# Kernel optimization log

Hardware: AMD Instinct MI355X
Metric: run time of the kernel (lower is better)

## Reference

```python
import jax, jax.numpy as jnp
import numpy as np

N = 100000
E = 2000000
LN_EPS = 1e-5


def _ln(x, g, b):
    m = jnp.mean(x, axis=-1, keepdims=True)
    v = jnp.mean((x - m) ** 2, axis=-1, keepdims=True)
    return (x - m) * jax.lax.rsqrt(v + LN_EPS) * g + b


def _gcn_conv(x, W, b, row, col, n_nodes):
    xw = x @ W  # [N, out_dim]
    deg = jax.ops.segment_sum(jnp.ones((row.shape[0],), xw.dtype), row, num_segments=n_nodes) + 1.0
    dinv = jax.lax.rsqrt(deg)
    norm = dinv[row] * dinv[col]  # [E]
    msg = xw[col] * norm[:, None]  # gather + scale, [E, out_dim]
    agg = jax.ops.segment_sum(msg, row, num_segments=n_nodes)
    self_loop = xw * (dinv * dinv)[:, None]
    return agg + self_loop + b


def setup_inputs() -> dict:
    key = jax.random.key(0)
    ks = jax.random.split(key, 32)
    s = 0.05
    d = dict(
        coords=jax.random.normal(ks[0], (N, 2), jnp.float32),
        features=jax.random.normal(ks[1], (N, 3), jnp.float32),
        edge_index=jax.random.randint(ks[2], (2, E), 0, N, jnp.int32),
        # spatial encoder FFN: 2->128, two hidden 128->128 (relu+LN), last 128->128 (relu)
        fw0=jax.random.normal(ks[3], (2, 128), jnp.float32) * s,
        fb0=jnp.zeros((128,), jnp.float32),
        fg0=jnp.ones((128,), jnp.float32),
        fe0=jnp.zeros((128,), jnp.float32),
        fw1=jax.random.normal(ks[4], (128, 128), jnp.float32) * s,
        fb1=jnp.zeros((128,), jnp.float32),
        fg1=jnp.ones((128,), jnp.float32),
        fe1=jnp.zeros((128,), jnp.float32),
        fw2=jax.random.normal(ks[5], (128, 128), jnp.float32) * s,
        fb2=jnp.zeros((128,), jnp.float32),
        fg2=jnp.ones((128,), jnp.float32),
        fe2=jnp.zeros((128,), jnp.float32),
        fw3=jax.random.normal(ks[6], (128, 128), jnp.float32) * s,
        fb3=jnp.zeros((128,), jnp.float32),
        # dec: 128->64->32->16 with tanh between
        dw0=jax.random.normal(ks[7], (128, 64), jnp.float32) * s,
        db0=jnp.zeros((64,), jnp.float32),
        dw1=jax.random.normal(ks[8], (64, 32), jnp.float32) * s,
        db1=jnp.zeros((32,), jnp.float32),
        dw2=jax.random.normal(ks[9], (32, 16), jnp.float32) * s,
        db2=jnp.zeros((16,), jnp.float32),
        # GCN convs: (3+16)->64, 64->64; fc 64->1
        cw1=jax.random.normal(ks[10], (19, 64), jnp.float32) * s,
        cb1=jnp.zeros((64,), jnp.float32),
        cw2=jax.random.normal(ks[11], (64, 64), jnp.float32) * s,
        cb2=jnp.zeros((64,), jnp.float32),
        ow=jax.random.normal(ks[12], (64, 1), jnp.float32) * s,
        ob=jnp.zeros((1,), jnp.float32),
    )
    return d


def reference(coords, features, edge_index,
              fw0, fb0, fg0, fe0, fw1, fb1, fg1, fe1, fw2, fb2, fg2, fe2, fw3, fb3,
              dw0, db0, dw1, db1, dw2, db2,
              cw1, cb1, cw2, cb2, ow, ob):
    # positional encoder FFN (dropout disabled / eval mode)
    h = _ln(jax.nn.relu(coords @ fw0 + fb0), fg0, fe0)
    h = _ln(jax.nn.relu(h @ fw1 + fb1), fg1, fe1)
    h = _ln(jax.nn.relu(h @ fw2 + fb2), fg2, fe2)
    h = jax.nn.relu(h @ fw3 + fb3)
    # decoder to emb_dim
    emb = jnp.tanh(h @ dw0 + db0)
    emb = jnp.tanh(emb @ dw1 + db1)
    emb = emb @ dw2 + db2  # [N, 16]
    x = jnp.concatenate([features, emb], axis=-1)  # [N, 19]
    row, col = edge_index[0], edge_index[1]
    h1 = jax.nn.relu(_gcn_conv(x, cw1, cb1, row, col, x.shape[0]))
    h2 = _gcn_conv(h1, cw2, cb2, row, col, x.shape[0])
    out = h2 @ ow + ob  # [N, 1]
    return out
```

## Files before the change

### kernel.cpp

```cpp
#include <hip/hip_runtime.h>
#include <hip/hip_bf16.h>
#include <math.h>

#define TM 64
#define XROW 64
#define NSEG 8

typedef float v2f __attribute__((ext_vector_type(2)));
typedef float f32x4 __attribute__((ext_vector_type(4)));
typedef __bf16 bf16x8 __attribute__((ext_vector_type(8)));
typedef unsigned short u16x8 __attribute__((ext_vector_type(8)));
typedef unsigned int uint_t;
typedef unsigned short ushort_t;

__device__ __forceinline__ v2f fma2(v2f a, v2f b, v2f c) {
    return __builtin_elementwise_fma(a, b, c);
}
__device__ __forceinline__ v2f splat2(float s) { return (v2f){s, s}; }
__device__ __forceinline__ v2f max02(v2f a) {
    return (v2f){fmaxf(a.x, 0.0f), fmaxf(a.y, 0.0f)};
}
__device__ __forceinline__ uint_t pack_bf16(float lo, float hi) {
    uint_t r;
    asm volatile("v_cvt_pk_bf16_f32 %0, %1, %2" : "=v"(r) : "v"(lo), "v"(hi));
    return r;
}
__device__ __forceinline__ float bf16_f(ushort_t u) {
    union { uint_t i; float f; } c; c.i = ((uint_t)u) << 16; return c.f;
}
__device__ __forceinline__ float blo(uint_t u) {
    union { uint_t i; float f; } c; c.i = u << 16; return c.f;
}
__device__ __forceinline__ float bhi(uint_t u) {
    union { uint_t i; float f; } c; c.i = u & 0xffff0000u; return c.f;
}

__device__ __forceinline__ int aaddr(int node, int feat) {
    return (node * 256 + feat * 2) ^ ((node & 15) << 4);
}

__global__ void prepw3_kernel(const float* __restrict__ W1, const float* __restrict__ W2,
                              const float* __restrict__ W3, ushort_t* __restrict__ out,
                              const float* __restrict__ cw2, const float* __restrict__ cb2,
                              const float* __restrict__ ow, const float* __restrict__ ob,
                              float* __restrict__ wb) {
    if (blockIdx.x == 384) {
        int i = threadIdx.x;
        if (i < 64) {
            float a = 0.f;
            for (int j = 0; j < 64; j++) a += cw2[i * 64 + j] * ow[j];
            wb[i] = a;
        }
        if (i == 0) {
            float bb = 0.f;
            for (int j = 0; j < 64; j++) bb += cb2[j] * ow[j];
            wb[64] = bb + ob[0];
        }
        return;
    }
    int gid = blockIdx.x * 256 + threadIdx.x;
    int layer = gid >> 15;
    int idx   = gid & 32767;
    const float* W = (layer == 0) ? W1 : (layer == 1) ? W2 : W3;
    int j    = idx & 7;
    int lane = (idx >> 3) & 63;
    int rest = idx >> 9;
    int cb   = rest & 7;
    int r2   = rest >> 3;
    int kk   = r2 & 3;
    int h    = r2 >> 2;
    int k = kk * 32 + (lane >> 4) * 8 + j;
    int n = cb * 16 + (lane & 15);
    float wv = W[k * 128 + n];
    ushort_t hi = (ushort_t)pack_bf16(wv, wv);
    ushort_t v;
    if (h == 0) v = hi;
    else {
        float res = wv - bf16_f(hi);
        v = (ushort_t)pack_bf16(res, res);
    }
    out[(size_t)layer * 32768 + idx] = v;
}

__global__ __launch_bounds__(256, 5) void ffn_kernel(
    const float* __restrict__ coords, const float* __restrict__ features,
    const float* __restrict__ dinv,
    const float* __restrict__ fw0, const float* __restrict__ fb0,
    const float* __restrict__ fg0, const float* __restrict__ fe0,
    const ushort_t* __restrict__ wswz,
    const float* __restrict__ fb1, const float* __restrict__ fg1, const float* __restrict__ fe1,
    const float* __restrict__ fb2, const float* __restrict__ fg2, const float* __restrict__ fe2,
    const float* __restrict__ fb3,
    const float* __restrict__ dw0, const float* __restrict__ db0,
    const float* __restrict__ dw1, const float* __restrict__ db1,
    const float* __restrict__ dw2, const float* __restrict__ db2,
    char* __restrict__ xsb, int n_nodes)
{
    __shared__ __align__(16) char abuf[16384];
    __shared__ __align__(16) ushort_t tbuf[128][64];

    const int t    = threadIdx.x;
    const int lane = t & 63;
    const int w    = __builtin_amdgcn_readfirstlane(t >> 6);
    const int jw   = w * 32;
    const int n0   = blockIdx.x * TM;

    int g = n0 + lane;
    if (g >= n_nodes) g = n_nodes - 1;

    {
        float* ps1 = (float*)tbuf;
        float* ps2 = ((float*)tbuf) + 256;
        v2f acc[16];
        float2 c = *(const float2*)&coords[(size_t)g * 2];
        v2f cx = splat2(c.x), cy = splat2(c.y);
        #pragma unroll
        for (int q = 0; q < 16; q++) {
            int j = jw + 2 * q;
            v2f w0 = *(const v2f*)&fw0[j];
            v2f w1 = *(const v2f*)&fw0[128 + j];
            v2f bb = *(const v2f*)&fb0[j];
            acc[q] = max02(fma2(cx, w0, fma2(cy, w1, bb)));
        }
        float s1 = 0.f, s2 = 0.f;
        #pragma unroll
        for (int q = 0; q < 16; q++) {
            s1 += acc[q].x + acc[q].y;
            s2 += acc[q].x * acc[q].x + acc[q].y * acc[q].y;
        }
        ps1[w * 64 + lane] = s1; ps2[w * 64 + lane] = s2;
        __syncthreads();
        float t1 = ps1[lane] + ps1[64 + lane] + ps1[128 + lane] + ps1[192 + lane];
        float t2 = ps2[lane] + ps2[64 + lane] + ps2[128 + lane] + ps2[192 + lane];
        float mean = t1 * (1.0f / 128.0f);
        float var  = t2 * (1.0f / 128.0f) - mean * mean;
        float inv  = rsqrtf(var + 1e-5f);
        v2f mean2 = splat2(mean), inv2 = splat2(inv);
        #pragma unroll
        for (int q = 0; q < 16; q++) {
            int j = jw + 2 * q;
            v2f gm = *(const v2f*)&fg0[j];
            v2f bt = *(const v2f*)&fe0[j];
            v2f o = fma2((acc[q] - mean2) * inv2, gm, bt);
            *(uint_t*)(abuf + aaddr(lane, j)) = pack_bf16(o.x, o.y);
        }
        __syncthreads();
    }

    auto mfma_layer = [&](const ushort_t* Wb, const float* __restrict__ bias) {
        f32x4 acc[2][4] = {};
        #pragma unroll
        for (int kk = 0; kk < 4; kk++) {
            bf16x8 B[2][2];
            #pragma unroll
            for (int cb2 = 0; cb2 < 2; cb2++) {
                int cb = 2 * w + cb2;
                #pragma unroll
                for (int h = 0; h < 2; h++) {
                    const ushort_t* p = Wb + (size_t)(((h * 4 + kk) * 8 + cb) * 64 + lane) * 8;
                    B[cb2][h] = *(const bf16x8*)p;
                }
            }
            #pragma unroll
            for (int rb = 0; rb < 4; rb++) {
                int node = rb * 16 + (lane & 15);
                bf16x8 A = *(const bf16x8*)(abuf + aaddr(node, kk * 32 + (lane >> 4) * 8));
                #pragma unroll
                for (int cb2 = 0; cb2 < 2; cb2++) {
                    acc[cb2][rb] = __builtin_amdgcn_mfma_f32_16x16x32_bf16(A, B[cb2][0], acc[cb2][rb], 0, 0, 0);
                    acc[cb2][rb] = __builtin_amdgcn_mfma_f32_16x16x32_bf16(A, B[cb2][1], acc[cb2][rb], 0, 0, 0);
                }
            }
        }
        __syncthreads();
        float bv0 = bias[jw + (lane & 15)];
        float bv1 = bias[jw + 16 + (lane & 15)];
        #pragma unroll
        for (int cb2 = 0; cb2 < 2; cb2++) {
            int col = jw + cb2 * 16 + (lane & 15);
            float bv = cb2 ? bv1 : bv0;
            #pragma unroll
            for (int rb = 0; rb < 4; rb++) {
                #pragma unroll
                for (int r = 0; r < 4; r++) {
                    float v = fmaxf(acc[cb2][rb][r] + bv, 0.0f);
                    int node = rb * 16 + (lane >> 4) * 4 + r;
                    *(ushort_t*)(abuf + aaddr(node, col)) = (ushort_t)pack_bf16(v, v);
                }
            }
        }
        __syncthreads();
    };

    auto ln_pass = [&](const float* __restrict__ gam, const float* __restrict__ bet) {
        int node = t >> 2;
        int part = t & 3;
        float vals[32];
        float s1 = 0.f, s2 = 0.f;
        #pragma unroll
        for (int q = 0; q < 4; q++) {
            int f0 = part * 32 + q * 8;
            u16x8 u = *(const u16x8*)(abuf + aaddr(node, f0));
            #pragma unroll
            for (int i = 0; i < 8; i++) {
                float v = bf16_f(u[i]);
                vals[q * 8 + i] = v;
                s1 += v; s2 += v * v;
            }
        }
        s1 += __shfl_xor(s1, 1); s1 += __shfl_xor(s1, 2);
        s2 += __shfl_xor(s2, 1); s2 += __shfl_xor(s2, 2);
        float mean = s1 * (1.0f / 128.0f);
        float var  = s2 * (1.0f / 128.0f) - mean * mean;
        float inv  = rsqrtf(var + 1e-5f);
        #pragma unroll
        for (int q = 0; q < 4; q++) {
            int f0 = part * 32 + q * 8;
            uint_t ov[4];
            #pragma unroll
            for (int p = 0; p < 4; p++) {
                v2f gm = *(const v2f*)&gam[f0 + 2 * p];
                v2f bt = *(const v2f*)&bet[f0 + 2 * p];
                float a = (vals[q * 8 + 2 * p]     - mean) * inv * gm.x + bt.x;
                float b = (vals[q * 8 + 2 * p + 1] - mean) * inv * gm.y + bt.y;
                ov[p] = pack_bf16(a, b);
            }
            uint4 uv = make_uint4(ov[0], ov[1], ov[2], ov[3]);
            *(uint4*)(abuf + aaddr(node, f0)) = uv;
        }
        __syncthreads();
    };

    mfma_layer(wswz,         fb1); ln_pass(fg1, fe1);
    mfma_layer(wswz + 32768, fb2); ln_pass(fg2, fe2);
    mfma_layer(wswz + 65536, fb3);

    {
        #pragma unroll
        for (int q = 0; q < 4; q++) {
            int f0 = jw + q * 8;
            u16x8 u = *(const u16x8*)(abuf + aaddr(lane, f0));
            #pragma unroll
            for (int i = 0; i < 8; i++) tbuf[f0 + i][lane] = u[i];
        }
        __syncthreads();
    }

    {
        const float2* src = (const float2*)dw0;
        uint_t* dst = (uint_t*)abuf;
        #pragma unroll
        for (int q = 0; q < 16; q++) {
            int i = q * 256 + t;
            float2 v = src[i];
            dst[i] = pack_bf16(v.x, v.y);
        }
        __syncthreads();
    }

    {
        const int j16 = w * 16;
        v2f d0[8];
        #pragma unroll
        for (int q = 0; q < 8; q++) d0[q] = *(const v2f*)&db0[j16 + 2 * q];
        const uint4* wd = (const uint4*)abuf;
        #pragma unroll 4
        for (int k = 0; k < 128; k++) {
            v2f av = splat2(bf16_f(tbuf[k][lane]));
            uint4 u0 = wd[k * 8 + w * 2];
            uint4 u1 = wd[k * 8 + w * 2 + 1];
            d0[0] = fma2(av, (v2f){blo(u0.x), bhi(u0.x)}, d0[0]);
            d0[1] = fma2(av, (v2f){blo(u0.y), bhi(u0.y)}, d0[1]);
            d0[2] = fma2(av, (v2f){blo(u0.z), bhi(u0.z)}, d0[2]);
            d0[3] = fma2(av, (v2f){blo(u0.w), bhi(u0.w)}, d0[3]);
            d0[4] = fma2(av, (v2f){blo(u1.x), bhi(u1.x)}, d0[4]);
            d0[5] = fma2(av, (v2f){blo(u1.y), bhi(u1.y)}, d0[5]);
            d0[6] = fma2(av, (v2f){blo(u1.z), bhi(u1.z)}, d0[6]);
            d0[7] = fma2(av, (v2f){blo(u1.w), bhi(u1.w)}, d0[7]);
        }
        #pragma unroll
        for (int q = 0; q < 8; q++) d0[q] = (v2f){tanhf(d0[q].x), tanhf(d0[q].y)};
        __syncthreads();
        #pragma unroll
        for (int q = 0; q < 8; q++) {
            uint_t r = pack_bf16(d0[q].x, d0[q].y);
            tbuf[j16 + 2 * q][lane]     = (ushort_t)r;
            tbuf[j16 + 2 * q + 1][lane] = (ushort_t)(r >> 16);
        }
        __syncthreads();
    }

    {
        const int j8 = w * 8;
        v2f d1[4];
        #pragma unroll
        for (int q = 0; q < 4; q++) d1[q] = *(const v2f*)&db1[j8 + 2 * q];
        #pragma unroll 4
        for (int k = 0; k < 64; k++) {
            v2f av = splat2(bf16_f(tbuf[k][lane]));
            const v2f* W2 = (const v2f*)(dw1 + k * 32 + j8);
            #pragma unroll
            for (int q = 0; q < 4; q++) d1[q] = fma2(av, W2[q], d1[q]);
        }
        #pragma unroll
        for (int q = 0; q < 4; q++) d1[q] = (v2f){tanhf(d1[q].x), tanhf(d1[q].y)};
        __syncthreads();
        #pragma unroll
        for (int q = 0; q < 4; q++) {
            uint_t r = pack_bf16(d1[q].x, d1[q].y);
            tbuf[j8 + 2 * q][lane]     = (ushort_t)r;
            tbuf[j8 + 2 * q + 1][lane] = (ushort_t)(r >> 16);
        }
        __syncthreads();
    }

    {
        const int j4 = w * 4;
        v2f d2[2];
        #pragma unroll
        for (int q = 0; q < 2; q++) d2[q] = *(const v2f*)&db2[j4 + 2 * q];
        #pragma unroll 4
        for (int k = 0; k < 32; k++) {
            v2f av = splat2(bf16_f(tbuf[k][lane]));
            const v2f* W2 = (const v2f*)(dw2 + k * 16 + j4);
            d2[0] = fma2(av, W2[0], d2[0]);
            d2[1] = fma2(av, W2[1], d2[1]);
        }
        __syncthreads();
        #pragma unroll
        for (int q = 0; q < 2; q++) {
            uint_t r = pack_bf16(d2[q].x, d2[q].y);
            tbuf[j4 + 2 * q][lane]     = (ushort_t)r;
            tbuf[j4 + 2 * q + 1][lane] = (ushort_t)(r >> 16);
        }
        __syncthreads();
    }

    {
        const int nn = t & 63;
        const int jg = t >> 6;
        int gg = n0 + nn;
        if (gg < n_nodes && jg < 3) {
            float dgg = dinv[gg];
            char* rp = xsb + (size_t)gg * XROW;
            if (jg == 0) {
                float4 f;
                f.x = features[(size_t)gg * 3 + 0] * dgg;
                f.y = features[(size_t)gg * 3 + 1] * dgg;
                f.z = features[(size_t)gg * 3 + 2] * dgg;
                f.w = 0.0f;
                *(float4*)rp = f;
            } else {
                int e0 = (jg - 1) * 8;
                uint_t u[4];
                #pragma unroll
                for (int p = 0; p < 4; p++) {
                    float lo = bf16_f(tbuf[e0 + 2 * p][nn]) * dgg;
                    float hi = bf16_f(tbuf[e0 + 2 * p + 1][nn]) * dgg;
                    u[p] = pack_bf16(lo, hi);
                }
                uint4 uv = make_uint4(u[0], u[1], u[2], u[3]);
                *(uint4*)(rp + 16 + (jg - 1) * 16) = uv;
            }
        }
    }
}

__global__ void deg8_kernel(const int* __restrict__ row, int* __restrict__ cnt8,
                            int E_, int Nn) {
    int s = blockIdx.x & (NSEG - 1);
    int* cs = cnt8 + (size_t)s * Nn;
    int e4 = (blockIdx.x * blockDim.x + threadIdx.x) * 4;
    if (e4 + 3 < E_) {
        int4 r = *(const int4*)&row[e4];
        atomicAdd(&cs[r.x], 1); atomicAdd(&cs[r.y], 1);
        atomicAdd(&cs[r.z], 1); atomicAdd(&cs[r.w], 1);
    } else {
        for (int e = e4; e < E_; e++) atomicAdd(&cs[row[e]], 1);
    }
}

__global__ void scan1_kernel(const int* __restrict__ in, int* __restrict__ out,
                             int* __restrict__ bsum, int n) {
    __shared__ int tmp[256];
    int t = threadIdx.x, b = blockIdx.x;
    int base = b * 2048 + t * 8;
    int v[8]; int s = 0;
    #pragma unroll
    for (int q = 0; q < 8; q++) {
        int idx = base + q;
        v[q] = (idx < n) ? in[idx] : 0;
        s += v[q];
    }
    tmp[t] = s; __syncthreads();
    #pragma unroll
    for (int d = 1; d < 256; d <<= 1) {
        int add = (t >= d) ? tmp[t - d] : 0;
        __syncthreads();
        tmp[t] += add;
        __syncthreads();
    }
    int run = tmp[t] - s;
    #pragma unroll
    for (int q = 0; q < 8; q++) {
        int idx = base + q;
        if (idx < n) out[idx] = run;
        run += v[q];
    }
    if (t == 255) bsum[b] = tmp[t];
}

__global__ void scan2_kernel(int* __restrict__ bsum, int B) {
    __shared__ int tmp[512];
    int t = threadIdx.x;
    tmp[t] = (t < B) ? bsum[t] : 0; __syncthreads();
    #pragma unroll
    for (int d = 1; d < 512; d <<= 1) {
        int add = (t >= d) ? tmp[t - d] : 0;
        __syncthreads();
        tmp[t] += add;
        __syncthreads();
    }
    if (t < B) bsum[t] = tmp[t];
}

__global__ void scanfix_dinv_kernel(int* __restrict__ data, const int* __restrict__ bsum,
                                    const int* __restrict__ cnt8, float* __restrict__ dinv,
                                    int n, int Nn) {
    int i = blockIdx.x * 256 + threadIdx.x;
    if (i < n) {
        int b = i >> 11;
        if (b > 0) data[i] += bsum[b - 1];
    }
    if (i < Nn) {
        int s = 0;
        #pragma unroll
        for (int q = 0; q < NSEG; q++) s += cnt8[(size_t)q * Nn + i];
        dinv[i] = rsqrtf((float)s + 1.0f);
    }
}

__global__ void scatter_kernel(const int* __restrict__ row, const int* __restrict__ col,
                               int* __restrict__ fill8, int* __restrict__ es,
                               int E_, int Nn) {
    int s = blockIdx.x & (NSEG - 1);
    int* fs = fill8 + (size_t)s * Nn;
    int e4 = (blockIdx.x * blockDim.x + threadIdx.x) * 4;
    if (e4 + 3 < E_) {
        int4 r = *(const int4*)&row[e4];
        int4 c = *(const int4*)&col[e4];
        es[atomicAdd(&fs[r.x], 1)] = c.x;
        es[atomicAdd(&fs[r.y], 1)] = c.y;
        es[atomicAdd(&fs[r.z], 1)] = c.z;
        es[atomicAdd(&fs[r.w], 1)] = c.w;
    } else {
        for (int e = e4; e < E_; e++) {
            int p = atomicAdd(&fs[row[e]], 1);
            es[p] = col[e];
        }
    }
}

__global__ __launch_bounds__(256) void node1g_kernel(
    const int* __restrict__ fill8, const int* __restrict__ cnt8, const int* __restrict__ es,
    const float* __restrict__ dinv, const char* __restrict__ xsb,
    const float* __restrict__ cw1, const float* __restrict__ cb1,
    const float* __restrict__ wb, float* __restrict__ ss, int n)
{
    __shared__ float w[19 * 64];
    __shared__ float bbs[64];
    __shared__ float wes[64];
    for (int i = threadIdx.x; i < 19 * 64; i += 256) w[i] = cw1[i];
    for (int i = threadIdx.x; i < 64; i += 256) { bbs[i] = cb1[i]; wes[i] = wb[i]; }
    __syncthreads();
    const int t  = threadIdx.x;
    const int oc = t & 7;
    const int i  = blockIdx.x * 32 + (t >> 3);
    if (i >= n) return;
    const float di = dinv[i];

    float af[19];
    #pragma unroll
    for (int q = 0; q < 19; q++) af[q] = 0.f;

    auto addrow = [&](const char* rp) {
        float4 F = *(const float4*)rp;
        uint4 U0 = *(const uint4*)(rp + 16);
        uint4 U1 = *(const uint4*)(rp + 32);
        af[0] += F.x; af[1] += F.y; af[2] += F.z;
        af[3]  += blo(U0.x); af[4]  += bhi(U0.x);
        af[5]  += blo(U0.y); af[6]  += bhi(U0.y);
        af[7]  += blo(U0.z); af[8]  += bhi(U0.z);
        af[9]  += blo(U0.w); af[10] += bhi(U0.w);
        af[11] += blo(U1.x); af[12] += bhi(U1.x);
        af[13] += blo(U1.y); af[14] += bhi(U1.y);
        af[15] += blo(U1.z); af[16] += bhi(U1.z);
        af[17] += blo(U1.w); af[18] += bhi(U1.w);
    };

    if (oc == 0) addrow(xsb + (size_t)i * XROW);
    const int end = fill8[(size_t)oc * n + i];
    const int dgs = cnt8[(size_t)oc * n + i];
    for (int e = end - dgs; e < end; e++) {
        int c = es[e];
        addrow(xsb + (size_t)c * XROW);
    }

    float a19[19];
    #pragma unroll
    for (int q = 0; q < 19; q++) {
        float v = af[q];
        v += __shfl_xor(v, 1);
        v += __shfl_xor(v, 2);
        v += __shfl_xor(v, 4);
        a19[q] = v * di;
    }

    const int j0 = oc * 8;
    v2f am[4];
    const v2f* w2  = (const v2f*)w;
    const v2f* bb2 = (const v2f*)bbs;
    #pragma unroll
    for (int q = 0; q < 4; q++) am[q] = bb2[j0 / 2 + q];
    #pragma unroll
    for (int k = 0; k < 19; k++) {
        v2f v = splat2(a19[k]);
        #pragma unroll
        for (int q = 0; q < 4; q++) am[q] = fma2(v, w2[k * 32 + j0 / 2 + q], am[q]);
    }
    const v2f* we2 = (const v2f*)wes;
    v2f sv2 = {0.f, 0.f};
    #pragma unroll
    for (int q = 0; q < 4; q++) sv2 = fma2(max02(am[q]), we2[j0 / 2 + q], sv2);
    float sv = sv2.x + sv2.y;
    sv += __shfl_xor(sv, 1);
    sv += __shfl_xor(sv, 2);
    sv += __shfl_xor(sv, 4);
    if (oc == 0) ss[i] = di * sv;
}

__global__ __launch_bounds__(256) void outg_kernel(
    const int* __restrict__ fill8, const int* __restrict__ cnt8, const int* __restrict__ es,
    const float* __restrict__ dinv, const float* __restrict__ ss,
    const float* __restrict__ wb, float* __restrict__ out, int n)
{
    const int t  = threadIdx.x;
    const int oc = t & 7;
    const int i  = blockIdx.x * 32 + (t >> 3);
    if (i >= n) return;
    const int end = fill8[(size_t)oc * n + i];
    const int dgs = cnt8[(size_t)oc * n + i];
    float sum = (oc == 0) ? ss[i] : 0.f;
    for (int e = end - dgs; e < end; e++) {
        int c = es[e];
        sum += ss[c];
    }
    sum += __shfl_xor(sum, 1);
    sum += __shfl_xor(sum, 2);
    sum += __shfl_xor(sum, 4);
    if (oc == 0) out[i] = wb[64] + dinv[i] * sum;
}

extern "C" void kernel_launch(void* const* d_in, const int* in_sizes, int n_in,
                              void* d_out, int out_size, void* d_ws, size_t ws_size,
                              hipStream_t stream) {
    const float* coords   = (const float*)d_in[0];
    const float* features = (const float*)d_in[1];
    const int*   eidx     = (const int*)d_in[2];
    const float* fw0 = (const float*)d_in[3];
    const float* fb0 = (const float*)d_in[4];
    const float* fg0 = (const float*)d_in[5];
    const float* fe0 = (const float*)d_in[6];
    const float* fw1 = (const float*)d_in[7];
    const float* fb1 = (const float*)d_in[8];
    const float* fg1 = (const float*)d_in[9];
    const float* fe1 = (const float*)d_in[10];
    const float* fw2 = (const float*)d_in[11];
    const float* fb2 = (const float*)d_in[12];
    const float* fg2 = (const float*)d_in[13];
    const float* fe2 = (const float*)d_in[14];
    const float* fw3 = (const float*)d_in[15];
    const float* fb3 = (const float*)d_in[16];
    const float* dw0 = (const float*)d_in[17];
    const float* db0 = (const float*)d_in[18];
    const float* dw1 = (const float*)d_in[19];
    const float* db1 = (const float*)d_in[20];
    const float* dw2 = (const float*)d_in[21];
    const float* db2 = (const float*)d_in[22];
    const float* cw1 = (const float*)d_in[23];
    const float* cb1 = (const float*)d_in[24];
    const float* cw2 = (const float*)d_in[25];
    const float* cb2 = (const float*)d_in[26];
    const float* ow  = (const float*)d_in[27];
    const float* ob  = (const float*)d_in[28];
    float* out = (float*)d_out;

    const int Nn = in_sizes[0] / 2;
    const int E_ = in_sizes[2] / 2;
    const int n8 = NSEG * Nn;
    const int NBS = (n8 + 2047) / 2048;
    const int NO = (Nn * 8 + 255) / 256;
    const int NT = (Nn + TM - 1) / TM;
    const int NE = (E_ / 4 + 255) / 256;

    char* ws = (char*)d_ws;
    size_t o = 0;
    char*  xsb   = (char*) (ws + o); o += (size_t)Nn * XROW;
    int*   cnt8  = (int*)  (ws + o); o += (size_t)n8 * sizeof(int);
    int*   fill8 = (int*)  (ws + o); o += (size_t)n8 * sizeof(int);
    int*   bsum  = (int*)  (ws + o); o += 512 * sizeof(int);
    float* dinv  = (float*)(ws + o); o += (size_t)Nn * sizeof(float);
    float* ssb   = (float*)(ws + o); o += (size_t)Nn * sizeof(float);
    int*   es    = (int*)  (ws + o); o += (size_t)E_ * sizeof(int);
    float* wb    = (float*)(ws + o); o += 80 * sizeof(float);
    o = (o + 15) & ~(size_t)15;
    ushort_t* wswz = (ushort_t*)(ws + o); o += 3 * 32768 * sizeof(ushort_t);

    hipMemsetAsync(cnt8, 0, (size_t)n8 * sizeof(int), stream);

    prepw3_kernel<<<385, 256, 0, stream>>>(fw1, fw2, fw3, wswz, cw2, cb2, ow, ob, wb);

    deg8_kernel<<<NE, 256, 0, stream>>>(eidx, cnt8, E_, Nn);
    scan1_kernel<<<NBS, 256, 0, stream>>>(cnt8, fill8, bsum, n8);
    scan2_kernel<<<1, 512, 0, stream>>>(bsum, NBS);
    scanfix_dinv_kernel<<<(n8 + 255) / 256, 256, 0, stream>>>(fill8, bsum, cnt8, dinv, n8, Nn);
    scatter_kernel<<<NE, 256, 0, stream>>>(eidx, eidx + E_, fill8, es, E_, Nn);

    ffn_kernel<<<NT, 256, 0, stream>>>(
        coords, features, dinv,
        fw0, fb0, fg0, fe0,
        wswz,
        fb1, fg1, fe1, fb2, fg2, fe2, fb3,
        dw0, db0,
        dw1, db1, dw2, db2, xsb, Nn);

    node1g_kernel<<<NO, 256, 0, stream>>>(fill8, cnt8, es, dinv, xsb, cw1, cb1, wb, ssb, Nn);
    outg_kernel<<<NO, 256, 0, stream>>>(fill8, cnt8, es, dinv, ssb, wb, out, Nn);
}
```

Before: 409.0 us.

## Merge independent kernels so degree/scatter blocks overlap weight prep and FFN

The degree-count kernel is folded into the weight-swizzle prep kernel, and the CSR scatter kernel is folded into the FFN kernel, with a block-index split choosing which role each block plays. This removes two launches and lets the atomic-bound edge work run alongside the MFMA-bound FFN tiles instead of serialising on the stream. The fused FFN kernel's launch bound drops from 5 to 4 blocks per CU, which may change register allocation and occupancy for the FFN path.

Result: faster. 375.0 us (median of 2 runs) (-8.3%).

```diff
diff --git a/kernel.cpp b/kernel.cpp
--- a/kernel.cpp
+++ b/kernel.cpp
@@ -39,12 +39,29 @@
     return (node * 256 + feat * 2) ^ ((node & 15) << 4);
 }
 
-__global__ void prepw3_kernel(const float* __restrict__ W1, const float* __restrict__ W2,
-                              const float* __restrict__ W3, ushort_t* __restrict__ out,
-                              const float* __restrict__ cw2, const float* __restrict__ cb2,
-                              const float* __restrict__ ow, const float* __restrict__ ob,
-                              float* __restrict__ wb) {
-    if (blockIdx.x == 384) {
+__global__ void deg8_prep_kernel(const int* __restrict__ row, int* __restrict__ cnt8,
+                                 int E_, int Nn, int NE,
+                                 const float* __restrict__ W1, const float* __restrict__ W2,
+                                 const float* __restrict__ W3, ushort_t* __restrict__ outw,
+                                 const float* __restrict__ cw2, const float* __restrict__ cb2,
+                                 const float* __restrict__ ow, const float* __restrict__ ob,
+                                 float* __restrict__ wb) {
+    int bid = blockIdx.x;
+    if (bid < NE) {
+        int s = bid & (NSEG - 1);
+        int* cs = cnt8 + (size_t)s * Nn;
+        int e4 = (bid * 256 + threadIdx.x) * 4;
+        if (e4 + 3 < E_) {
+            int4 r = *(const int4*)&row[e4];
+            atomicAdd(&cs[r.x], 1); atomicAdd(&cs[r.y], 1);
+            atomicAdd(&cs[r.z], 1); atomicAdd(&cs[r.w], 1);
+        } else {
+            for (int e = e4; e < E_; e++) atomicAdd(&cs[row[e]], 1);
+        }
+        return;
+    }
+    int pid = bid - NE;
+    if (pid == 384) {
         int i = threadIdx.x;
         if (i < 64) {
             float a = 0.f;
@@ -58,7 +75,7 @@
         }
         return;
     }
-    int gid = blockIdx.x * 256 + threadIdx.x;
+    int gid = pid * 256 + threadIdx.x;
     int layer = gid >> 15;
     int idx   = gid & 32767;
     const float* W = (layer == 0) ? W1 : (layer == 1) ? W2 : W3;
@@ -79,10 +96,12 @@
         float res = wv - bf16_f(hi);
         v = (ushort_t)pack_bf16(res, res);
     }
-    out[(size_t)layer * 32768 + idx] = v;
-}
-
-__global__ __launch_bounds__(256, 5) void ffn_kernel(
+    outw[(size_t)layer * 32768 + idx] = v;
+}
+
+__global__ __launch_bounds__(256, 4) void scatter_ffn_kernel(
+    const int* __restrict__ row, const int* __restrict__ col,
+    int* __restrict__ fill8, int* __restrict__ es, int E_, int NE,
     const float* __restrict__ coords, const float* __restrict__ features,
     const float* __restrict__ dinv,
     const float* __restrict__ fw0, const float* __restrict__ fb0,
@@ -99,11 +118,34 @@
     __shared__ __align__(16) char abuf[16384];
     __shared__ __align__(16) ushort_t tbuf[128][64];
 
-    const int t    = threadIdx.x;
+    const int bid = blockIdx.x;
+    const int t   = threadIdx.x;
+
+    if (bid < NE) {
+        int s = bid & (NSEG - 1);
+        int Nn = n_nodes;
+        int* fs = fill8 + (size_t)s * Nn;
+        int e4 = (bid * 256 + t) * 4;
+        if (e4 + 3 < E_) {
+            int4 r = *(const int4*)&row[e4];
+            int4 c = *(const int4*)&col[e4];
+            es[atomicAdd(&fs[r.x], 1)] = c.x;
+            es[atomicAdd(&fs[r.y], 1)] = c.y;
+            es[atomicAdd(&fs[r.z], 1)] = c.z;
+            es[atomicAdd(&fs[r.w], 1)] = c.w;
+        } else {
+            for (int e = e4; e < E_; e++) {
+                int p = atomicAdd(&fs[row[e]], 1);
+                es[p] = col[e];
+            }
+        }
+        return;
+    }
+
     const int lane = t & 63;
     const int w    = __builtin_amdgcn_readfirstlane(t >> 6);
     const int jw   = w * 32;
-    const int n0   = blockIdx.x * TM;
+    const int n0   = (bid - NE) * TM;
 
     int g = n0 + lane;
     if (g >= n_nodes) g = n_nodes - 1;
@@ -177,7 +219,7 @@
         float bv1 = bias[jw + 16 + (lane & 15)];
         #pragma unroll
         for (int cb2 = 0; cb2 < 2; cb2++) {
-            int col = jw + cb2 * 16 + (lane & 15);
+            int col2 = jw + cb2 * 16 + (lane & 15);
             float bv = cb2 ? bv1 : bv0;
             #pragma unroll
             for (int rb = 0; rb < 4; rb++) {
@@ -185,7 +227,7 @@
                 for (int r = 0; r < 4; r++) {
                     float v = fmaxf(acc[cb2][rb][r] + bv, 0.0f);
                     int node = rb * 16 + (lane >> 4) * 4 + r;
-                    *(ushort_t*)(abuf + aaddr(node, col)) = (ushort_t)pack_bf16(v, v);
+                    *(ushort_t*)(abuf + aaddr(node, col2)) = (ushort_t)pack_bf16(v, v);
                 }
             }
         }
@@ -366,20 +408,6 @@
     }
 }
 
-__global__ void deg8_kernel(const int* __restrict__ row, int* __restrict__ cnt8,
-                            int E_, int Nn) {
-    int s = blockIdx.x & (NSEG - 1);
-    int* cs = cnt8 + (size_t)s * Nn;
-    int e4 = (blockIdx.x * blockDim.x + threadIdx.x) * 4;
-    if (e4 + 3 < E_) {
-        int4 r = *(const int4*)&row[e4];
-        atomicAdd(&cs[r.x], 1); atomicAdd(&cs[r.y], 1);
-        atomicAdd(&cs[r.z], 1); atomicAdd(&cs[r.w], 1);
-    } else {
-        for (int e = e4; e < E_; e++) atomicAdd(&cs[row[e]], 1);
-    }
-}
-
 __global__ void scan1_kernel(const int* __restrict__ in, int* __restrict__ out,
                              int* __restrict__ bsum, int n) {
     __shared__ int tmp[256];
@@ -437,27 +465,6 @@
         #pragma unroll
         for (int q = 0; q < NSEG; q++) s += cnt8[(size_t)q * Nn + i];
         dinv[i] = rsqrtf((float)s + 1.0f);
-    }
-}
-
-__global__ void scatter_kernel(const int* __restrict__ row, const int* __restrict__ col,
-                               int* __restrict__ fill8, int* __restrict__ es,
-                               int E_, int Nn) {
-    int s = blockIdx.x & (NSEG - 1);
-    int* fs = fill8 + (size_t)s * Nn;
-    int e4 = (blockIdx.x * blockDim.x + threadIdx.x) * 4;
-    if (e4 + 3 < E_) {
-        int4 r = *(const int4*)&row[e4];
-        int4 c = *(const int4*)&col[e4];
-        es[atomicAdd(&fs[r.x], 1)] = c.x;
-        es[atomicAdd(&fs[r.y], 1)] = c.y;
-        es[atomicAdd(&fs[r.z], 1)] = c.z;
-        es[atomicAdd(&fs[r.w], 1)] = c.w;
-    } else {
-        for (int e = e4; e < E_; e++) {
-            int p = atomicAdd(&fs[row[e]], 1);
-            es[p] = col[e];
-        }
     }
 }
 
@@ -618,21 +625,20 @@
 
     hipMemsetAsync(cnt8, 0, (size_t)n8 * sizeof(int), stream);
 
-    prepw3_kernel<<<385, 256, 0, stream>>>(fw1, fw2, fw3, wswz, cw2, cb2, ow, ob, wb);
-
-    deg8_kernel<<<NE, 256, 0, stream>>>(eidx, cnt8, E_, Nn);
+    deg8_prep_kernel<<<NE + 385, 256, 0, stream>>>(eidx, cnt8, E_, Nn, NE,
+                                                   fw1, fw2, fw3, wswz,
+                                                   cw2, cb2, ow, ob, wb);
     scan1_kernel<<<NBS, 256, 0, stream>>>(cnt8, fill8, bsum, n8);
     scan2_kernel<<<1, 512, 0, stream>>>(bsum, NBS);
     scanfix_dinv_kernel<<<(n8 + 255) / 256, 256, 0, stream>>>(fill8, bsum, cnt8, dinv, n8, Nn);
-    scatter_kernel<<<NE, 256, 0, stream>>>(eidx, eidx + E_, fill8, es, E_, Nn);
-
-    ffn_kernel<<<NT, 256, 0, stream>>>(
+
+    scatter_ffn_kernel<<<NE + NT, 256, 0, stream>>>(
+        eidx, eidx + E_, fill8, es, E_, NE,
         coords, features, dinv,
         fw0, fb0, fg0, fe0,
         wswz,
         fb1, fg1, fe1, fb2, fg2, fe2, fb3,
-        dw0, db0,
-        dw1, db1, dw2, db2, xsb, Nn);
+        dw0, db0, dw1, db1, dw2, db2, xsb, Nn);
 
     node1g_kernel<<<NO, 256, 0, stream>>>(fill8, cnt8, es, dinv, xsb, cw1, cb1, wb, ssb, Nn);
     outg_kernel<<<NO, 256, 0, stream>>>(fill8, cnt8, es, dinv, ssb, wb, out, Nn);
```
